# Kernel optimization log

Measured on AMD Instinct MI355X. Metric: run time of the kernel, lower is better.

The kernel has to match this reference:

```python
import jax, jax.numpy as jnp
import numpy as np
import math

B, N, DIM, H = 4, 2048, 1024, 16
DH = DIM // H

def setup_inputs() -> dict:
    key = jax.random.key(0)
    ks = jax.random.split(key, 7)
    return {
        "x": jax.random.normal(ks[0], (B, N, DIM), dtype=jnp.float32),
        "qkv_w": jax.random.normal(ks[1], (3 * DIM, DIM), dtype=jnp.float32) * 0.02,
        "qkv_b": jax.random.normal(ks[2], (3 * DIM,), dtype=jnp.float32) * 0.02,
        "proj_w": jax.random.normal(ks[3], (DIM, DIM), dtype=jnp.float32) * 0.02,
        "proj_b": jax.random.normal(ks[4], (DIM,), dtype=jnp.float32) * 0.02,
        "temperature": jnp.ones((1,), dtype=jnp.float32) * 0.1,
        "eps": jax.random.normal(ks[5], (B, H, N, DH), dtype=jnp.float32),
    }

def reference(x, qkv_w, qkv_b, proj_w, proj_b, temperature, eps):
    b, n, dim = x.shape
    qkv = x @ qkv_w.T + qkv_b
    qkv = qkv.reshape(b, n, 3, H, DH).transpose(2, 0, 3, 1, 4)
    q, k, v = qkv[0], qkv[1], qkv[2]
    # quantum fluctuation: additive gaussian noise on q, scaled by sigmoid(temperature)
    q = q + eps * jax.nn.sigmoid(temperature)
    scale = 1.0 / math.sqrt(DH)
    attn = jnp.einsum("bhqd,bhkd->bhqk", q, k) * scale  # [B,H,N,N]
    attn = jax.nn.softmax(attn, axis=-1)
    out = jnp.einsum("bhqk,bhkd->bhqd", attn, v)  # [B,H,N,DH]
    out = out.transpose(0, 2, 1, 3).reshape(b, n, dim)
    return out @ proj_w.T + proj_b
```

## Files before the change

### kernel.cpp

```cpp
#include <hip/hip_runtime.h>
#include <math.h>

#define B_   4
#define N_   2048
#define DIM_ 1024
#define H_   16
#define DH_  64
#define M_   (B_ * N_)
#define QKV_ELEMS ((size_t)B_ * H_ * N_ * DH_)

typedef __attribute__((ext_vector_type(8))) short short8;
typedef __attribute__((ext_vector_type(4))) float floatx4;

static __device__ inline unsigned short f2bf(float f) {
    union { float f; unsigned u; } v; v.f = f;
    unsigned r = (v.u + 0x7fffu + ((v.u >> 16) & 1u)) >> 16;
    return (unsigned short)r;
}

static __device__ inline unsigned pkbf(float a, float b) {
    unsigned ua = (__float_as_uint(a) + 0x8000u) >> 16;
    unsigned ub = (__float_as_uint(b) + 0x8000u) & 0xffff0000u;
    return ua | ub;
}

static __device__ inline void async_copy16(const void* g, void* l) {
    __builtin_amdgcn_global_load_lds(
        (const __attribute__((address_space(1))) unsigned int*)g,
        (__attribute__((address_space(3))) unsigned int*)l, 16, 0, 0);
}

__global__ __launch_bounds__(256) void f32_to_bf16_kernel(
    const float* __restrict__ src, unsigned short* __restrict__ dst, int n8)
{
    int i = blockIdx.x * 256 + threadIdx.x;
    if (i >= n8) return;
    float4 a = ((const float4*)src)[i * 2];
    float4 b = ((const float4*)src)[i * 2 + 1];
    short8 o;
    o[0] = f2bf(a.x); o[1] = f2bf(a.y); o[2] = f2bf(a.z); o[3] = f2bf(a.w);
    o[4] = f2bf(b.x); o[5] = f2bf(b.y); o[6] = f2bf(b.z); o[7] = f2bf(b.w);
    *(short8*)(dst + (size_t)i * 8) = o;
}

#define GEMM_BODY(Aptr, Bptr, K)                                               \
    __shared__ unsigned short As[128 * 32];                                    \
    __shared__ unsigned short Bs[128 * 32];                                    \
    const int tid  = threadIdx.x;                                              \
    const int lane = tid & 63;                                                 \
    const int wv   = tid >> 6;                                                 \
    const int l15  = lane & 15, quad = lane >> 4;                              \
    const int wrow = (wv >> 1) * 64, wcol = (wv & 1) * 64;                     \
    const int m0 = blockIdx.y * 128, n0 = blockIdx.x * 128;                    \
    const int lrow = lane >> 2;                                                \
    const int lkc  = (lane & 3) * 8;                                           \
    const unsigned short* ga0 = Aptr + (size_t)(m0 + wv * 32 + lrow) * K + lkc;\
    const unsigned short* ga1 = ga0 + (size_t)16 * K;                          \
    const unsigned short* gb0 = Bptr + (size_t)(n0 + wv * 32 + lrow) * K + lkc;\
    const unsigned short* gb1 = gb0 + (size_t)16 * K;                          \
    unsigned short* lA0 = &As[wv * 1024];                                      \
    unsigned short* lA1 = lA0 + 512;                                           \
    unsigned short* lB0 = &Bs[wv * 1024];                                      \
    unsigned short* lB1 = lB0 + 512;                                           \
    floatx4 acc[4][4] = {};                                                    \
    for (int k0 = 0; k0 < K; k0 += 32) {                                       \
        __syncthreads();                                                       \
        async_copy16(ga0 + k0, lA0);                                           \
        async_copy16(ga1 + k0, lA1);                                           \
        async_copy16(gb0 + k0, lB0);                                           \
        async_copy16(gb1 + k0, lB1);                                           \
        __syncthreads();                                                       \
        short8 af[4], bf[4];                                                   \
        _Pragma("unroll")                                                      \
        for (int mt = 0; mt < 4; ++mt)                                         \
            af[mt] = *(const short8*)&As[(wrow + mt * 16 + l15) * 32 + quad * 8];\
        _Pragma("unroll")                                                      \
        for (int nt = 0; nt < 4; ++nt)                                         \
            bf[nt] = *(const short8*)&Bs[(wcol + nt * 16 + l15) * 32 + quad * 8];\
        _Pragma("unroll")                                                      \
        for (int mt = 0; mt < 4; ++mt)                                         \
            _Pragma("unroll")                                                  \
            for (int nt = 0; nt < 4; ++nt)                                     \
                acc[mt][nt] = __builtin_amdgcn_mfma_f32_16x16x32_bf16(         \
                    af[mt], bf[nt], acc[mt][nt], 0, 0, 0);                     \
    }

__global__ __launch_bounds__(256) void gemm_qkv_bf16(
    const unsigned short* __restrict__ A, const unsigned short* __restrict__ Bm,
    const float* __restrict__ bias, const float* __restrict__ eps,
    const float* __restrict__ temp,
    unsigned short* __restrict__ qb, unsigned short* __restrict__ kb,
    unsigned short* __restrict__ vb)
{
    GEMM_BODY(A, Bm, 1024)

    const float sig = 1.0f / (1.0f + __expf(-temp[0]));
    const float qscale = 0.125f * 1.44269504f;
#pragma unroll
    for (int mt = 0; mt < 4; ++mt) {
#pragma unroll
        for (int r = 0; r < 4; ++r) {
            const int m  = m0 + wrow + mt * 16 + quad * 4 + r;
            const int b  = m >> 11;
            const int nn = m & 2047;
#pragma unroll
            for (int nt = 0; nt < 4; ++nt) {
                const int n = n0 + wcol + nt * 16 + l15;
                float val = acc[mt][nt][r] + bias[n];
                const int which = n >> 10;
                const int d  = n & 1023;
                const int h  = d >> 6;
                const int dd = d & 63;
                const size_t bh = (size_t)(b * H_ + h);
                if (which == 0) {
                    const size_t idx = (bh * N_ + nn) * DH_ + dd;
                    qb[idx] = f2bf((val + eps[idx] * sig) * qscale);
                } else if (which == 1) {
                    kb[(bh * N_ + nn) * DH_ + dd] = f2bf(val);
                } else {
                    vb[(bh * DH_ + dd) * N_ + nn] = f2bf(val);
                }
            }
        }
    }
}

__global__ __launch_bounds__(256) void gemm_proj_bf16(
    const unsigned short* __restrict__ A, const unsigned short* __restrict__ Bm,
    const float* __restrict__ bias, float* __restrict__ out)
{
    GEMM_BODY(A, Bm, 1024)

#pragma unroll
    for (int mt = 0; mt < 4; ++mt) {
#pragma unroll
        for (int r = 0; r < 4; ++r) {
            const int m = m0 + wrow + mt * 16 + quad * 4 + r;
#pragma unroll
            for (int nt = 0; nt < 4; ++nt) {
                const int n = n0 + wcol + nt * 16 + l15;
                out[(size_t)m * 1024 + n] = acc[mt][nt][r] + bias[n];
            }
        }
    }
}

__global__ __launch_bounds__(256, 2) void attn_kernel(
    const unsigned short* __restrict__ qb, const unsigned short* __restrict__ kb,
    const unsigned short* __restrict__ vt, unsigned short* __restrict__ attn_out)
{
    const int tid  = threadIdx.x;
    const int lane = tid & 63;
    const int wv   = tid >> 6;
    const int l15  = lane & 15;
    const int quad = lane >> 4;
    const int q1   = quad >> 1;
    const int q0b  = quad & 1;

    const int f  = blockIdx.x;
    const int L  = (f & 7) * 64 + (f >> 3);
    const int bh = L >> 3;
    const int b  = bh >> 4, h = bh & 15;
    const int qbase = (L & 7) * 256 + wv * 64;

    const unsigned short* kb_bh = kb + (size_t)bh * N_ * DH_;
    const unsigned short* vt_bh = vt + (size_t)bh * DH_ * N_;

    short8 qf[4][2];
#pragma unroll
    for (int g = 0; g < 4; ++g) {
        const unsigned short* qp =
            qb + ((size_t)bh * N_ + qbase + g * 16 + l15) * DH_;
        qf[g][0] = *(const short8*)(qp + quad * 8);
        qf[g][1] = *(const short8*)(qp + 32 + quad * 8);
    }

    floatx4 o[4][4] = {};
    float l_part[4] = {0.f, 0.f, 0.f, 0.f};

    const unsigned short* kA = kb_bh + (size_t)l15 * DH_ + quad * 8;
    const unsigned short* vA = vt_bh + (size_t)l15 * N_ + quad * 8;

    short8 kfA[2][2], kfB[2][2];

#define LOADK(DST, ktn)                                                        \
    do {                                                                       \
        _Pragma("unroll")                                                      \
        for (int nt = 0; nt < 2; ++nt) {                                       \
            _Pragma("unroll")                                                  \
            for (int hh = 0; hh < 2; ++hh)                                     \
                DST[nt][hh] = *(const short8*)(                                \
                    kA + (size_t)((ktn) * 32 + nt * 16) * DH_ + hh * 32);      \
        }                                                                      \
    } while (0)

#define TILE(CUR, NXT, kt, ktn)                                                \
    do {                                                                       \
        short8 vf[4];                                                          \
        _Pragma("unroll")                                                      \
        for (int dt = 0; dt < 4; ++dt)                                         \
            vf[dt] = *(const short8*)(vA + (size_t)dt * 16 * N_ + (kt) * 32);  \
        LOADK(NXT, ktn);                             \
        _Pragma("unroll")                                                      \
        for (int g = 0; g < 4; ++g) {                                          \
            floatx4 s0 = {}, s1 = {};                                          \
            __builtin_amdgcn_s_setprio(1);                                     \
            s0 = __builtin_amdgcn_mfma_f32_16x16x32_bf16(CUR[0][0], qf[g][0], s0, 0, 0, 0); \
            s0 = __builtin_amdgcn_mfma_f32_16x16x32_bf16(CUR[0][1], qf[g][1], s0, 0, 0, 0); \
            s1 = __builtin_amdgcn_mfma_f32_16x16x32_bf16(CUR[1][0], qf[g][0], s1, 0, 0, 0); \
            s1 = __builtin_amdgcn_mfma_f32_16x16x32_bf16(CUR[1][1], qf[g][1], s1, 0, 0, 0); \
            __builtin_amdgcn_s_setprio(0);                                     \
            _Pragma("unroll")                                                  \
            for (int r = 0; r < 4; ++r) {                                      \
                s0[r] = __builtin_amdgcn_exp2f(s0[r]);                         \
                s1[r] = __builtin_amdgcn_exp2f(s1[r]);                         \
            }                                                                  \
            l_part[g] += ((s0[0] + s0[1]) + (s0[2] + s0[3]))                   \
                       + ((s1[0] + s1[1]) + (s1[2] + s1[3]));                  \
                           \
            unsigned w0 = pkbf(s0[0], s0[1]);                                  \
            unsigned w1 = pkbf(s0[2], s0[3]);                                  \
            unsigned w2 = pkbf(s1[0], s1[1]);                                  \
            unsigned w3 = pkbf(s1[2], s1[3]);                                  \
                  \
            unsigned t0 = q1 ? w0 : w2, t1 = q1 ? w1 : w3;                     \
            unsigned r0 = (unsigned)__shfl_xor((int)t0, 32, 64);               \
            unsigned r1 = (unsigned)__shfl_xor((int)t1, 32, 64);               \
            unsigned m0 = q1 ? r0 : w0, m1 = q1 ? r1 : w1;                     \
            unsigned m2 = q1 ? w2 : r0, m3 = q1 ? w3 : r1;                     \
                  \
            unsigned u0 = q0b ? m0 : m2, u1 = q0b ? m1 : m3;                   \
            unsigned x0 = (unsigned)__shfl_xor((int)u0, 16, 64);               \
            unsigned x1 = (unsigned)__shfl_xor((int)u1, 16, 64);               \
            union { unsigned u[4]; short8 s8; } pu;                            \
            pu.u[0] = q0b ? x0 : m0; pu.u[1] = q0b ? x1 : m1;                  \
            pu.u[2] = q0b ? m2 : x0; pu.u[3] = q0b ? m3 : x1;                  \
            const short8 pf = pu.s8;    \
            __builtin_amdgcn_s_setprio(1);                                     \
            _Pragma("unroll")                                                  \
            for (int dt = 0; dt < 4; ++dt)                                     \
                o[g][dt] = __builtin_amdgcn_mfma_f32_16x16x32_bf16(            \
                    pf, vf[dt], o[g][dt], 0, 0, 0);                            \
            __builtin_amdgcn_s_setprio(0);                                     \
        }                                                                      \
    } while (0)

    LOADK(kfA, 0);
    for (int kt = 0; kt < 64; kt += 2) {
        TILE(kfA, kfB, kt, kt + 1);
        TILE(kfB, kfA, kt + 1, (kt + 2 < 64) ? (kt + 2) : 0);
    }
#undef TILE
#undef LOADK

#pragma unroll
    for (int g = 0; g < 4; ++g) {
        float lsum = l_part[g];
        lsum += __shfl_xor(lsum, 16, 64);
        lsum += __shfl_xor(lsum, 32, 64);
        const float inv = 1.0f / lsum;
#pragma unroll
        for (int r = 0; r < 4; ++r) {
            const float invq = __shfl(inv, quad * 4 + r, 64);
            const int row = qbase + g * 16 + quad * 4 + r;
#pragma unroll
            for (int dt = 0; dt < 4; ++dt)
                attn_out[((size_t)b * N_ + row) * DIM_ + h * DH_ + dt * 16 + l15] =
                    f2bf(o[g][dt][r] * invq);
        }
    }
}

extern "C" void kernel_launch(void* const* d_in, const int* in_sizes, int n_in,
                              void* d_out, int out_size, void* d_ws, size_t ws_size,
                              hipStream_t stream) {
    const float* x      = (const float*)d_in[0];
    const float* qkv_w  = (const float*)d_in[1];
    const float* qkv_b  = (const float*)d_in[2];
    const float* proj_w = (const float*)d_in[3];
    const float* proj_b = (const float*)d_in[4];
    const float* temp   = (const float*)d_in[5];
    const float* eps    = (const float*)d_in[6];
    float* out = (float*)d_out;

    unsigned short* qb   = (unsigned short*)d_ws;
    unsigned short* kb   = qb + QKV_ELEMS;
    unsigned short* vb   = kb + QKV_ELEMS;
    unsigned short* xb   = vb + QKV_ELEMS;
    unsigned short* wqb  = xb + QKV_ELEMS;
    unsigned short* pwb  = wqb + (size_t)3 * DIM_ * DIM_;
    unsigned short* attn = pwb + (size_t)DIM_ * DIM_;

    dim3 blk(256);
    f32_to_bf16_kernel<<<dim3(8388608 / 8 / 256), blk, 0, stream>>>(x, xb, 8388608 / 8);
    f32_to_bf16_kernel<<<dim3(3145728 / 8 / 256), blk, 0, stream>>>(qkv_w, wqb, 3145728 / 8);
    f32_to_bf16_kernel<<<dim3(1048576 / 8 / 256), blk, 0, stream>>>(proj_w, pwb, 1048576 / 8);

    gemm_qkv_bf16<<<dim3(24, 64), blk, 0, stream>>>(xb, wqb, qkv_b, eps, temp,
                                                    qb, kb, vb);
    attn_kernel<<<dim3(512), dim3(256), 0, stream>>>(qb, kb, vb, attn);
    gemm_proj_bf16<<<dim3(8, 64), blk, 0, stream>>>(attn, pwb, proj_b, out);
}
```

Before: 395.5 us.

## Pre-permute V layout to drop P shuffles and software-pipeline QK with PV

The QKV GEMM epilogue now writes V in a permuted tiled layout matching the MFMA output register layout of P. This lets the attention kernel feed exp'd scores straight into the PV MFMA without the cross-lane shuffles and selects it used before. The inner loop is also restructured so the QK MFMAs for the next query group are issued alongside the softmax/PV of the current one, with K and V double-buffered in registers. This adds register pressure and a final wasted QK, and it depends on the permuted V indexing being exactly right.

```diff
diff --git a/kernel.cpp b/kernel.cpp
--- a/kernel.cpp
+++ b/kernel.cpp
@@ -118,7 +118,13 @@
                 } else if (which == 1) {
                     kb[(bh * N_ + nn) * DH_ + dd] = f2bf(val);
                 } else {
-                    vb[(bh * DH_ + dd) * N_ + nn] = f2bf(val);
+                    const int kt  = nn >> 5;
+                    const int k32 = nn & 31;
+                    const int lo  = k32 & 15;
+                    const int a   = lo >> 2;
+                    const int j   = ((k32 >> 4) << 2) + (lo & 3);
+                    vb[bh * (size_t)(N_ * DH_) +
+                       ((size_t)(kt * 64 + dd) * 4 + a) * 8 + j] = f2bf(val);
                 }
             }
         }
@@ -154,8 +160,6 @@
     const int wv   = tid >> 6;
     const int l15  = lane & 15;
     const int quad = lane >> 4;
-    const int q1   = quad >> 1;
-    const int q0b  = quad & 1;
 
     const int f  = blockIdx.x;
     const int L  = (f & 7) * 64 + (f >> 3);
@@ -164,7 +168,7 @@
     const int qbase = (L & 7) * 256 + wv * 64;
 
     const unsigned short* kb_bh = kb + (size_t)bh * N_ * DH_;
-    const unsigned short* vt_bh = vt + (size_t)bh * DH_ * N_;
+    const unsigned short* vt_bh = vt + (size_t)bh * N_ * DH_;
 
     short8 qf[4][2];
 #pragma unroll
@@ -179,79 +183,80 @@
     float l_part[4] = {0.f, 0.f, 0.f, 0.f};
 
     const unsigned short* kA = kb_bh + (size_t)l15 * DH_ + quad * 8;
-    const unsigned short* vA = vt_bh + (size_t)l15 * N_ + quad * 8;
-
-    short8 kfA[2][2], kfB[2][2];
+
+    short8 kfA[2][2], kfB[2][2], vfA[4], vfB[4];
+    floatx4 sa0, sa1, sb0, sb1;
 
 #define LOADK(DST, ktn)                                                        \
     do {                                                                       \
         _Pragma("unroll")                                                      \
-        for (int nt = 0; nt < 2; ++nt) {                                       \
+        for (int nt = 0; nt < 2; ++nt)                                         \
             _Pragma("unroll")                                                  \
             for (int hh = 0; hh < 2; ++hh)                                     \
                 DST[nt][hh] = *(const short8*)(                                \
                     kA + (size_t)((ktn) * 32 + nt * 16) * DH_ + hh * 32);      \
+    } while (0)
+
+#define LOADV(DST, ktn)                                                        \
+    do {                                                                       \
+        _Pragma("unroll")                                                      \
+        for (int dt = 0; dt < 4; ++dt)                                         \
+            DST[dt] = *(const short8*)(vt_bh +                                 \
+                ((size_t)((ktn) * 64 + dt * 16 + l15) * 4 + quad) * 8);        \
+    } while (0)
+
+#define QK(S0, S1, KF, g)                                                      \
+    do {                                                                       \
+        floatx4 z0 = {}, z1 = {};                                              \
+        z0 = __builtin_amdgcn_mfma_f32_16x16x32_bf16(KF[0][0], qf[g][0], z0, 0, 0, 0); \
+        z0 = __builtin_amdgcn_mfma_f32_16x16x32_bf16(KF[0][1], qf[g][1], z0, 0, 0, 0); \
+        z1 = __builtin_amdgcn_mfma_f32_16x16x32_bf16(KF[1][0], qf[g][0], z1, 0, 0, 0); \
+        z1 = __builtin_amdgcn_mfma_f32_16x16x32_bf16(KF[1][1], qf[g][1], z1, 0, 0, 0); \
+        S0 = z0; S1 = z1;                                                      \
+    } while (0)
+
+#define SPV(S0, S1, VF, g)                                                     \
+    do {                                                                       \
+        _Pragma("unroll")                                                      \
+        for (int r = 0; r < 4; ++r) {                                          \
+            S0[r] = __builtin_amdgcn_exp2f(S0[r]);                             \
+            S1[r] = __builtin_amdgcn_exp2f(S1[r]);                             \
         }                                                                      \
+        l_part[g] += ((S0[0] + S0[1]) + (S0[2] + S0[3]))                       \
+                   + ((S1[0] + S1[1]) + (S1[2] + S1[3]));                      \
+        union { unsigned u[4]; short8 s8; } pu;                                \
+        pu.u[0] = pkbf(S0[0], S0[1]); pu.u[1] = pkbf(S0[2], S0[3]);            \
+        pu.u[2] = pkbf(S1[0], S1[1]); pu.u[3] = pkbf(S1[2], S1[3]);            \
+        o[g][0] = __builtin_amdgcn_mfma_f32_16x16x32_bf16(pu.s8, VF[0], o[g][0], 0, 0, 0); \
+        o[g][1] = __builtin_amdgcn_mfma_f32_16x16x32_bf16(pu.s8, VF[1], o[g][1], 0, 0, 0); \
+        o[g][2] = __builtin_amdgcn_mfma_f32_16x16x32_bf16(pu.s8, VF[2], o[g][2], 0, 0, 0); \
+        o[g][3] = __builtin_amdgcn_mfma_f32_16x16x32_bf16(pu.s8, VF[3], o[g][3], 0, 0, 0); \
     } while (0)
 
-#define TILE(CUR, NXT, kt, ktn)                                                \
-    do {                                                                       \
-        short8 vf[4];                                                          \
-        _Pragma("unroll")                                                      \
-        for (int dt = 0; dt < 4; ++dt)                                         \
-            vf[dt] = *(const short8*)(vA + (size_t)dt * 16 * N_ + (kt) * 32);  \
-        LOADK(NXT, ktn);                             \
-        _Pragma("unroll")                                                      \
-        for (int g = 0; g < 4; ++g) {                                          \
-            floatx4 s0 = {}, s1 = {};                                          \
-            __builtin_amdgcn_s_setprio(1);                                     \
-            s0 = __builtin_amdgcn_mfma_f32_16x16x32_bf16(CUR[0][0], qf[g][0], s0, 0, 0, 0); \
-            s0 = __builtin_amdgcn_mfma_f32_16x16x32_bf16(CUR[0][1], qf[g][1], s0, 0, 0, 0); \
-            s1 = __builtin_amdgcn_mfma_f32_16x16x32_bf16(CUR[1][0], qf[g][0], s1, 0, 0, 0); \
-            s1 = __builtin_amdgcn_mfma_f32_16x16x32_bf16(CUR[1][1], qf[g][1], s1, 0, 0, 0); \
-            __builtin_amdgcn_s_setprio(0);                                     \
-            _Pragma("unroll")                                                  \
-            for (int r = 0; r < 4; ++r) {                                      \
-                s0[r] = __builtin_amdgcn_exp2f(s0[r]);                         \
-                s1[r] = __builtin_amdgcn_exp2f(s1[r]);                         \
-            }                                                                  \
-            l_part[g] += ((s0[0] + s0[1]) + (s0[2] + s0[3]))                   \
-                       + ((s1[0] + s1[1]) + (s1[2] + s1[3]));                  \
-                           \
-            unsigned w0 = pkbf(s0[0], s0[1]);                                  \
-            unsigned w1 = pkbf(s0[2], s0[3]);                                  \
-            unsigned w2 = pkbf(s1[0], s1[1]);                                  \
-            unsigned w3 = pkbf(s1[2], s1[3]);                                  \
-                  \
-            unsigned t0 = q1 ? w0 : w2, t1 = q1 ? w1 : w3;                     \
-            unsigned r0 = (unsigned)__shfl_xor((int)t0, 32, 64);               \
-            unsigned r1 = (unsigned)__shfl_xor((int)t1, 32, 64);               \
-            unsigned m0 = q1 ? r0 : w0, m1 = q1 ? r1 : w1;                     \
-            unsigned m2 = q1 ? w2 : r0, m3 = q1 ? w3 : r1;                     \
-                  \
-            unsigned u0 = q0b ? m0 : m2, u1 = q0b ? m1 : m3;                   \
-            unsigned x0 = (unsigned)__shfl_xor((int)u0, 16, 64);               \
-            unsigned x1 = (unsigned)__shfl_xor((int)u1, 16, 64);               \
-            union { unsigned u[4]; short8 s8; } pu;                            \
-            pu.u[0] = q0b ? x0 : m0; pu.u[1] = q0b ? x1 : m1;                  \
-            pu.u[2] = q0b ? m2 : x0; pu.u[3] = q0b ? m3 : x1;                  \
-            const short8 pf = pu.s8;    \
-            __builtin_amdgcn_s_setprio(1);                                     \
-            _Pragma("unroll")                                                  \
-            for (int dt = 0; dt < 4; ++dt)                                     \
-                o[g][dt] = __builtin_amdgcn_mfma_f32_16x16x32_bf16(            \
-                    pf, vf[dt], o[g][dt], 0, 0, 0);                            \
-            __builtin_amdgcn_s_setprio(0);                                     \
-        }                                                                      \
-    } while (0)
-
-    LOADK(kfA, 0);
+    LOADK(kfA, 0); LOADV(vfA, 0);
+    LOADK(kfB, 1); LOADV(vfB, 1);
+    QK(sa0, sa1, kfA, 0);
+
     for (int kt = 0; kt < 64; kt += 2) {
-        TILE(kfA, kfB, kt, kt + 1);
-        TILE(kfB, kfA, kt + 1, (kt + 2 < 64) ? (kt + 2) : 0);
-    }
-#undef TILE
+        const int t2 = (kt + 2) & 63;
+        const int t3 = (kt + 3) & 63;
+        QK(sb0, sb1, kfA, 1);  SPV(sa0, sa1, vfA, 0);
+        QK(sa0, sa1, kfA, 2);  SPV(sb0, sb1, vfA, 1);
+        QK(sb0, sb1, kfA, 3);  SPV(sa0, sa1, vfA, 2);
+        LOADK(kfA, t2);
+        QK(sa0, sa1, kfB, 0);  SPV(sb0, sb1, vfA, 3);
+        LOADV(vfA, t2);
+        QK(sb0, sb1, kfB, 1);  SPV(sa0, sa1, vfB, 0);
+        QK(sa0, sa1, kfB, 2);  SPV(sb0, sb1, vfB, 1);
+        QK(sb0, sb1, kfB, 3);  SPV(sa0, sa1, vfB, 2);
+        LOADK(kfB, t3);
+        QK(sa0, sa1, kfA, 0);  SPV(sb0, sb1, vfB, 3);
+        LOADV(vfB, t3);
+    }
+#undef QK
+#undef SPV
 #undef LOADK
+#undef LOADV
 
 #pragma unroll
     for (int g = 0; g < 4; ++g) {
```

Result: faster. 386.5 us (-2.3%).
